# Kernel tuning notes

Measured on AMD Instinct MI355X. Metric: run time of the kernel, lower is better.

Reference implementation:

```python
import jax, jax.numpy as jnp
import numpy as np

HEADS = 4
DIM_K = 16
DIM_U = 1
EPS = 1e-5


def _rel_pos_idx(n):
    # torch: meshgrid(ij) -> stack -> '(i j) n'; rel = pos[None,:]-pos[:,None] + n-1
    ii, jj = np.meshgrid(np.arange(n), np.arange(n), indexing='ij')
    pos = np.stack([ii, jj]).reshape(2, -1).T  # (n*n, 2)
    rel = pos[None, :] - pos[:, None] + (n - 1)  # (N, N, 2)
    return rel[..., 0], rel[..., 1]


def _bn(t, gamma, beta):
    # BatchNorm2d in training mode: batch stats over (b, h, w), biased var
    mu = t.mean(axis=(0, 1, 2))
    var = t.var(axis=(0, 1, 2))
    return (t - mu) * jax.lax.rsqrt(var + EPS) * gamma + beta


def setup_inputs() -> dict:
    key = jax.random.key(0)
    ks = jax.random.split(key, 16)
    b, n, c = 8, 48, 128
    hk = DIM_K * HEADS          # 64
    v = 128 // HEADS            # 32 (dim_out // heads)
    rl = 2 * n - 1              # 95
    s = 0.02
    return {
        'x': jax.random.normal(ks[0], (b, n, n, c), jnp.float32),
        'cor': jax.random.normal(ks[1], (b, n, n, 2), jnp.float32),
        'Wq': jax.random.normal(ks[2], (hk, c), jnp.float32) * s,
        'Wk': jax.random.normal(ks[3], (DIM_K * DIM_U, c), jnp.float32) * s,
        'Wv': jax.random.normal(ks[4], (v * DIM_U, c), jnp.float32) * s,
        'Wce': jax.random.normal(ks[5], (hk, 2), jnp.float32) * s,
        'bce': jax.random.normal(ks[6], (hk,), jnp.float32) * s,
        'Wcc': jax.random.normal(ks[7], (hk, 128), jnp.float32) * s,
        'Wmp': jax.random.normal(ks[8], (128, hk), jnp.float32) * s,
        'bmp': jax.random.normal(ks[9], (128,), jnp.float32) * s,
        'gq': jnp.ones((hk,), jnp.float32),
        'bq': jnp.zeros((hk,), jnp.float32),
        'gv': jnp.ones((v * DIM_U,), jnp.float32),
        'bv': jnp.zeros((v * DIM_U,), jnp.float32),
        'rel_pos_emb': jax.random.normal(ks[10], (rl, rl, DIM_K, DIM_U), jnp.float32),
    }


def reference(x, cor, Wq, Wk, Wv, Wce, bce, Wcc, Wmp, bmp, gq, bq, gv, bv, rel_pos_emb):
    b, hh, ww, c = x.shape
    h, u, kd = HEADS, DIM_U, DIM_K
    vd = Wv.shape[0] // u
    N = hh * ww

    # frame reversal along batch
    x_rev = jnp.concatenate([x[b // 2:], x[:b // 2]], axis=0)

    # 1x1 convs as channel matmuls (channels-last)
    q = jnp.einsum('bhwc,oc->bhwo', x, Wq)
    k = jnp.einsum('bhwc,oc->bhwo', x_rev, Wk)
    v = jnp.einsum('bhwc,oc->bhwo', x_rev, Wv)

    Qn = _bn(q, gq, bq)
    Vn = _bn(v, gv, bv)

    Q = jnp.transpose(Qn.reshape(b, N, h, kd), (0, 2, 3, 1))       # b h k n
    K = jnp.transpose(k.reshape(b, N, u, kd), (0, 2, 3, 1))        # b u k m
    V = jnp.transpose(Vn.reshape(b, N, u, vd), (0, 2, 3, 1))       # b u v m

    K = jax.nn.softmax(K, axis=-1)
    lamc = jnp.einsum('bukm,buvm->bkv', K, V)
    Yc = jnp.einsum('bhkn,bkv->bhvn', Q, lamc)

    # relative position lambda (global branch)
    ni, mi = _rel_pos_idx(hh)
    emb = rel_pos_emb[ni, mi]                                      # n m k u
    lamp = jnp.einsum('nmku,buvm->bnkv', emb, V)
    Yp = jnp.einsum('bhkn,bnkv->bhvn', Q, lamp)

    Y = Yc + Yp                                                    # b h v n
    appearance = jnp.transpose(Y.reshape(b, h, vd, hh, ww), (0, 3, 4, 1, 2)).reshape(b, hh, ww, h * vd)

    cor_embed_ = jnp.einsum('bhwc,oc->bhwo', cor, Wce) + bce       # b hh ww (h k)
    cor_embed = jnp.transpose(cor_embed_.reshape(b, N, h, kd), (0, 2, 3, 1))  # b h k n
    crc = jnp.einsum('bhkn,bkv->bhvn', cor_embed, lamc)
    crp = jnp.einsum('bhkn,bnkv->bhvn', cor_embed, lamp)
    cor_reverse_ = jnp.transpose((crc + crp).reshape(b, h, vd, hh, ww), (0, 3, 4, 1, 2)).reshape(b, hh, ww, h * vd)
    cor_reverse = jnp.einsum('bhwc,oc->bhwo', cor_reverse_, Wcc)
    motion = jnp.einsum('bhwc,oc->bhwo', cor_reverse - cor_embed_, Wmp) + bmp
    return appearance, motion
```

## Files before the change

### kernel.cpp

```cpp
#include <hip/hip_runtime.h>
#include <math.h>
#include <stdint.h>

#define NNPOS 2304
#define ROWS  18432
#define NK    96

#define O_Q   0ul
#define O_K   1179648ul
#define O_V   1474560ul
#define O_ST  2064384ul
#define O_VP  2064704ul
#define O_QP  2457920ul
#define O_LC  4817216ul
#define O_RT  6000960ul
#define O_WG  6148416ul
#define O_B2  6148672ul
#define O_WB  6148800ul
#define O_PT  6155968ul
#define O_PV  6164160ul
#define O_PE  6166208ul
#define O_WFB 6167232ul
#define O_CRF 6175424ul

typedef __bf16 bf16x8 __attribute__((ext_vector_type(8)));
typedef float  f32x4  __attribute__((ext_vector_type(4)));
typedef unsigned int u32;
typedef u32 u32x4 __attribute__((ext_vector_type(4)));

__global__ void k_fold(const float* __restrict__ Wcc, const float* __restrict__ Wce,
                       const float* __restrict__ Wmp, const float* __restrict__ bmp,
                       const float* __restrict__ bce, const float* __restrict__ Wq,
                       const float* __restrict__ Wk, const float* __restrict__ Wv,
                       float* __restrict__ ws) {
  const int t = threadIdx.x;
  const int g = blockIdx.x * 256 + t;
  const int o2 = g >> 7, c = g & 127;
  float acc = 0.f;
#pragma unroll 8
  for (int o = 0; o < 64; ++o) acc += Wmp[o2 * 64 + o] * Wcc[o * 128 + c];
  ((__bf16*)(ws + O_WFB))[o2 * 128 + c] = (__bf16)acc;
  if (blockIdx.x == 0 && t < 128) {
    float a0 = 0.f, a1 = 0.f, ab = 0.f;
#pragma unroll 8
    for (int o = 0; o < 64; ++o) {
      float w = Wmp[t * 64 + o];
      a0 += w * Wce[o * 2]; a1 += w * Wce[o * 2 + 1]; ab += w * bce[o];
    }
    ws[O_WG + t * 2] = a0; ws[O_WG + t * 2 + 1] = a1; ws[O_B2 + t] = bmp[t] - ab;
  }
  __bf16* wbp = (__bf16*)(ws + O_WB);
  if (g < 14336) {
    float w;
    if (g < 8192) w = Wq[g];
    else if (g < 10240) w = Wk[g - 8192];
    else w = Wv[g - 10240];
    wbp[g] = (__bf16)w;
  }
}

__global__ __launch_bounds__(256) void k_qkv(const float* __restrict__ x,
                                             float* __restrict__ ws) {
  const int t = threadIdx.x;
  const int wave = t >> 6, lane = t & 63;
  const int lr = lane & 15, quad = lane >> 4;
  const int r0 = blockIdx.x * 64 + wave * 16;
  const int b = r0 / NNPOS;
  const int n0 = r0 - b * NNPOS;
  const size_t outbase = (size_t)(((b + 4) & 7)) * NNPOS + n0;

  const __bf16* wb = (const __bf16*)(ws + O_WB);
  const float* xrow = x + (size_t)(r0 + lr) * 128;

  f32x4 acc[7];
#pragma unroll
  for (int i = 0; i < 7; ++i) acc[i] = (f32x4){0.f, 0.f, 0.f, 0.f};

#pragma unroll
  for (int ks = 0; ks < 4; ++ks) {
    const float* ap = xrow + ks * 32 + quad * 8;
    float4 a0 = *(const float4*)(ap);
    float4 a1 = *(const float4*)(ap + 4);
    bf16x8 af;
    af[0] = (__bf16)a0.x; af[1] = (__bf16)a0.y; af[2] = (__bf16)a0.z; af[3] = (__bf16)a0.w;
    af[4] = (__bf16)a1.x; af[5] = (__bf16)a1.y; af[6] = (__bf16)a1.z; af[7] = (__bf16)a1.w;
#pragma unroll
    for (int ct = 0; ct < 7; ++ct) {
      bf16x8 bfrag = *(const bf16x8*)(wb + (ct * 16 + lr) * 128 + ks * 32 + quad * 8);
      acc[ct] = __builtin_amdgcn_mfma_f32_16x16x32_bf16(af, bfrag, acc[ct], 0, 0, 0);
    }
  }

#pragma unroll
  for (int ct = 0; ct < 7; ++ct) {
#pragma unroll
    for (int reg = 0; reg < 4; ++reg) {
      int m = quad * 4 + reg;
      int oc = ct * 16 + lr;
      float vvv = acc[ct][reg];
      if (ct < 4)      ws[O_Q + (size_t)(r0 + m) * 64 + oc] = vvv;
      else if (ct < 5) ws[O_K + (outbase + m) * 16 + (oc - 64)] = vvv;
      else             ws[O_V + (outbase + m) * 32 + (oc - 80)] = vvv;
    }
  }
}

__global__ void k_rt(const float* __restrict__ rel, float* __restrict__ ws) {
  __bf16* rt = (__bf16*)(ws + O_RT);
  int i = blockIdx.x * 256 + threadIdx.x;
  if (i < 144400) {
    int kc = i & 15, rr = i >> 4;
    int ri = rr / 95, rj = rr - ri * 95;
    rt[(size_t)kc * 9216 + ri * 96 + rj] = (__bf16)rel[i];
  }
}

__global__ void k_zero(float* __restrict__ ws) {
  __bf16* vp = (__bf16*)(ws + O_VP);
  int i = blockIdx.x * 256 + threadIdx.x;
  if (i < 4096) ws[O_LC + i] = 0.f;
  int bv = i / 96, rem = i - bv * 96;
  int mi = rem >> 1, h8 = rem & 1;
  uint4 z; z.x = 0; z.y = 0; z.z = 0; z.w = 0;
  *(uint4*)(vp + (size_t)bv * 3072 + mi * 64 + 48 + h8 * 8) = z;
}

__global__ void k_zout(float* __restrict__ out, float* __restrict__ ws) {
  size_t i = (size_t)blockIdx.x * 256 + threadIdx.x;
  f32x4 z = {0.f, 0.f, 0.f, 0.f};
  ((f32x4*)out)[i] = z;
  ((f32x4*)(ws + O_CRF))[i] = z;
}

__global__ void k_stats1(float* __restrict__ ws) {
  const int t = threadIdx.x, blk = blockIdx.x;
  __shared__ float sh[512];
  if (blk < 64) {
    const int ch = t & 63, rsub = t >> 6;
    const float* src = ws + O_Q;
    const int r0 = blk * 288;
    float s = 0.f, s2 = 0.f;
#pragma unroll 4
    for (int i = 0; i < 72; ++i) {
      float v = src[(size_t)(r0 + rsub + i * 4) * 64 + ch];
      s += v; s2 += v * v;
    }
    sh[t] = s; sh[256 + t] = s2;
    __syncthreads();
    if (t < 64) {
      float S = sh[t] + sh[t + 64] + sh[t + 128] + sh[t + 192];
      float S2 = sh[256 + t] + sh[256 + t + 64] + sh[256 + t + 128] + sh[256 + t + 192];
      ws[O_PT + blk * 128 + t * 2] = S; ws[O_PT + blk * 128 + t * 2 + 1] = S2;
    }
  } else if (blk < 96) {
    const int j = blk - 64;
    const int ch = t & 31, rsub = t >> 5;
    const float* src = ws + O_V;
    const int r0 = j * 576;
    float s = 0.f, s2 = 0.f;
#pragma unroll 4
    for (int i = 0; i < 72; ++i) {
      float v = src[(size_t)(r0 + rsub + i * 8) * 32 + ch];
      s += v; s2 += v * v;
    }
    sh[t] = s; sh[256 + t] = s2;
    __syncthreads();
    if (t < 32) {
      float S = 0.f, S2 = 0.f;
#pragma unroll
      for (int k = 0; k < 8; ++k) { S += sh[t + k * 32]; S2 += sh[256 + t + k * 32]; }
      ws[O_PV + j * 64 + t * 2] = S; ws[O_PV + j * 64 + t * 2 + 1] = S2;
    }
  } else {
    const int idx = blk - 96;
    const int b = idx >> 3, sl = idx & 7;
    const int kc = t & 15, rsub = t >> 4;
    const int r0 = b * 2304 + sl * 288;
    float s = 0.f;
#pragma unroll 2
    for (int i = 0; i < 18; ++i)
      s += __expf(ws[O_K + (size_t)(r0 + rsub + i * 16) * 16 + kc]);
    sh[t] = s;
    __syncthreads();
    if (t < 16) {
      float S = 0.f;
#pragma unroll
      for (int k = 0; k < 16; ++k) S += sh[t + k * 16];
      ws[O_PE + b * 128 + sl * 16 + t] = S;
    }
  }
}

__global__ void k_stats2(const float* __restrict__ gq, const float* __restrict__ bq,
                         const float* __restrict__ gv, const float* __restrict__ bv,
                         float* __restrict__ ws) {
  const int t = threadIdx.x;
  if (t < 64) {
    float S = 0.f, S2 = 0.f;
    for (int i = 0; i < 64; ++i) { S += ws[O_PT + i * 128 + t * 2]; S2 += ws[O_PT + i * 128 + t * 2 + 1]; }
    float mu = S / 18432.f, var = S2 / 18432.f - mu * mu;
    float sc = gq[t] * rsqrtf(var + 1e-5f);
    ws[O_ST + t] = sc; ws[O_ST + 64 + t] = bq[t] - mu * sc;
  } else if (t < 96) {
    int ch = t - 64;
    float S = 0.f, S2 = 0.f;
    for (int i = 0; i < 32; ++i) { S += ws[O_PV + i * 64 + ch * 2]; S2 += ws[O_PV + i * 64 + ch * 2 + 1]; }
    float mu = S / 18432.f, var = S2 / 18432.f - mu * mu;
    float sc = gv[ch] * rsqrtf(var + 1e-5f);
    ws[O_ST + 128 + ch] = sc; ws[O_ST + 160 + ch] = bv[ch] - mu * sc;
  } else if (t < 224) {
    int idx = t - 96; int b = idx >> 4, kc = idx & 15;
    float S = 0.f;
#pragma unroll
    for (int sl = 0; sl < 8; ++sl) S += ws[O_PE + b * 128 + sl * 16 + kc];
    ws[O_ST + 192 + idx] = 1.f / S;
  }
}

__global__ void k_vp(float* __restrict__ ws) {
  const int b = blockIdx.x / 48, mi = blockIdx.x - b * 48;
  const int t = threadIdx.x;
  __shared__ float Vn[48 * 33];
  const float* st = ws + O_ST;
  const int r0 = b * 2304 + mi * 48;
#pragma unroll
  for (int i = t; i < 1536; i += 256) {
    int r = i >> 5, j = i & 31;
    Vn[r * 33 + j] = ws[O_V + (size_t)(r0 + r) * 32 + j] * st[128 + j] + st[160 + j];
  }
  __syncthreads();
  __bf16* vp = (__bf16*)(ws + O_VP);
  const int j = t >> 3, seg = t & 7;
  unsigned short u[6];
#pragma unroll
  for (int q = 0; q < 6; ++q)
    u[q] = __builtin_bit_cast(unsigned short, (__bf16)Vn[(seg * 6 + q) * 33 + j]);
  u32 w0 = (u32)u[0] | ((u32)u[1] << 16);
  u32 w1 = (u32)u[2] | ((u32)u[3] << 16);
  u32 w2 = (u32)u[4] | ((u32)u[5] << 16);
  u32* dst = (u32*)(vp + (size_t)(b * 32 + j) * 3072 + mi * 64 + seg * 6);
  dst[0] = w0; dst[1] = w1; dst[2] = w2;
}

__global__ void k_prep(const float* __restrict__ cor, const float* __restrict__ Wce,
                       const float* __restrict__ bce, float* __restrict__ ws) {
  const int t = threadIdx.x;
  const int rl = t >> 5, j = t & 31;
  const int rid = blockIdx.x * 8 + rl;
  const int b = rid / NNPOS, n = rid - b * NNPOS;
  const float* st = ws + O_ST;
  float c0 = cor[rid * 2], c1 = cor[rid * 2 + 1];
#pragma unroll
  for (int ch = j; ch < 64; ch += 32) {
    float qn = ws[O_Q + (size_t)rid * 64 + ch] * st[ch] + st[64 + ch];
    ws[O_QP + (size_t)(n * 8 + b) * 128 + ch] = qn;
    float ce = c0 * Wce[ch * 2] + c1 * Wce[ch * 2 + 1] + bce[ch];
    ws[O_QP + (size_t)(n * 8 + b) * 128 + 64 + ch] = ce;
  }
}

__global__ void k_lamc(float* __restrict__ ws) {
  const int b = blockIdx.x / 36, sl = blockIdx.x - b * 36;
  const int t = threadIdx.x;
  __shared__ float eK[16][16];
  __shared__ float Vn[16][33];
  const float* st = ws + O_ST;
  const int kc = t & 15, vp_ = t >> 4;
  const int v0 = vp_ * 2, v1 = v0 + 1;
  float a0 = 0.f, a1 = 0.f;
  const int m0 = b * 2304 + sl * 64;
  const int jj = t & 31, rw = t >> 5;
  const float scj = st[128 + jj], bij = st[160 + jj];
  for (int ch = 0; ch < 4; ++ch) {
    const int mbase = m0 + ch * 16;
    eK[t >> 4][t & 15] = __expf(ws[O_K + (size_t)(mbase + (t >> 4)) * 16 + (t & 15)]);
    Vn[rw][jj]     = ws[O_V + (size_t)(mbase + rw) * 32 + jj] * scj + bij;
    Vn[rw + 8][jj] = ws[O_V + (size_t)(mbase + rw + 8) * 32 + jj] * scj + bij;
    __syncthreads();
#pragma unroll
    for (int m = 0; m < 16; ++m) {
      float e = eK[m][kc];
      a0 += e * Vn[m][v0];
      a1 += e * Vn[m][v1];
    }
    __syncthreads();
  }
  atomicAdd(&ws[O_LC + (size_t)(b * 16 + kc) * 32 + v0], a0);
  atomicAdd(&ws[O_LC + (size_t)(b * 16 + kc) * 32 + v1], a1);
}

__global__ __launch_bounds__(256, 2) void k_lamp(float* __restrict__ ws,
                                                 float* __restrict__ out) {
  __shared__ __align__(16) char smem[33792];
  bf16x8* Bs16 = (bf16x8*)smem;
  u32* Sw = (u32*)(smem + 8192);
  float* Cs = (float*)smem;

  const int t = threadIdx.x;
  const int bx = blockIdx.x;
  const int ni = bx / 6;
  const int sset = bx - ni * 6;
  const int s0 = (sset < 3) ? sset * 16 : (sset - 3) * 16 + 1;
  const int chalf = blockIdx.y;
  const int khalf = blockIdx.z;
  const int ks0 = khalf * 48, ksE = ks0 + 48;
  const int colbase = chalf * 128;
  const int wave = t >> 6, lane = t & 63;
  const int wrow = wave >> 1, wcol = wave & 1;
  const int lr = lane & 15, quad = lane >> 4;

  const __bf16* vp = (const __bf16*)(ws + O_VP);
  const unsigned short* rp = (const unsigned short*)(ws + O_RT);

  const int ia0 = t;
  const int kcA0 = ia0 / 24, wpA0 = ia0 - kcA0 * 24;
  const int ia1 = t + 256;
  const int kcA1 = ia1 / 24, wpA1 = ia1 - kcA1 * 24;
  const bool hasA1 = (ia1 < 384);

  const int colB0 = t >> 2, pB0 = ((t & 3) - ((t >> 3) & 3)) & 3;
  const int ub1 = t + 256;
  const int colB1 = ub1 >> 2, pB1 = ((ub1 & 3) - ((ub1 >> 3) & 3)) & 3;
  const __bf16* gB0 = vp + (size_t)(colbase + colB0) * 3072 + pB0 * 8;
  const __bf16* gB1 = vp + (size_t)(colbase + colB1) * 3072 + pB1 * 8;

  f32x4 acc[4][4];
  {
    f32x4 zz = {0.f, 0.f, 0.f, 0.f};
#pragma unroll
    for (int i = 0; i < 4; ++i)
#pragma unroll
      for (int j = 0; j < 4; ++j) acc[i][j] = zz;
  }

  u32 sa0 = 0, sa1 = 0;
  bf16x8 vb0, vb1;

  auto loadStep = [&](int ksn) {
    const int mi = ksn >> 1, mj0 = (ksn & 1) << 5;
    const int P0 = 96 * (mi - ni + 47) + mj0 - s0 + 33;
    const int k0 = ksn * 32;
    long b0 = (long)kcA0 * 9216 + P0 + 2 * wpA0;
    if (P0 & 1) sa0 = (u32)rp[b0] | ((u32)rp[b0 + 1] << 16);
    else        sa0 = *(const u32*)(rp + b0);
    if (hasA1) {
      long b1 = (long)kcA1 * 9216 + P0 + 2 * wpA1;
      if (P0 & 1) sa1 = (u32)rp[b1] | ((u32)rp[b1 + 1] << 16);
      else        sa1 = *(const u32*)(rp + b1);
    }
    vb0 = *(const bf16x8*)(gB0 + k0);
    vb1 = *(const bf16x8*)(gB1 + k0);
  };

  loadStep(ks0);

  for (int ks = ks0; ks < ksE; ++ks) {
    __syncthreads();
    Sw[kcA0 * 25 + wpA0] = sa0;
    if (hasA1) Sw[kcA1 * 25 + wpA1] = sa1;
    Bs16[t] = vb0;
    Bs16[t + 256] = vb1;
    __syncthreads();

    if (ks + 1 < ksE) loadStep(ks + 1);

    bf16x8 af[4], bfr[4];
#pragma unroll
    for (int rt = 0; rt < 4; ++rt) {
      int nl = wrow * 4 + rt;
      int wb = lr * 25 + (7 - nl) + quad * 4;
      u32x4 dd = { Sw[wb], Sw[wb + 1], Sw[wb + 2], Sw[wb + 3] };
      af[rt] = __builtin_bit_cast(bf16x8, dd);
    }
#pragma unroll
    for (int ct = 0; ct < 4; ++ct) {
      int col = wcol * 64 + ct * 16 + lr;
      int u = col * 4 + ((quad + (col >> 1)) & 3);
      bfr[ct] = Bs16[u];
    }
#pragma unroll
    for (int rt = 0; rt < 4; ++rt)
#pragma unroll
      for (int ct = 0; ct < 4; ++ct)
        acc[rt][ct] = __builtin_amdgcn_mfma_f32_16x16x32_bf16(af[rt], bfr[ct], acc[rt][ct], 0, 0, 0);
  }

  const float* lamcp = ws + O_LC;
  const float* Qp = ws + O_QP;
  float* crf = ws + O_CRF;
  const int s = t >> 5, vv = t & 31;

  for (int h = 0; h < 2; ++h) {
    __syncthreads();
    if (wrow == h) {
#pragma unroll
      for (int rt = 0; rt < 4; ++rt) {
#pragma unroll
        for (int ct = 0; ct < 4; ++ct) {
          int col = wcol * 64 + ct * 16 + lr;
          int bb = chalf * 4 + (col >> 5);
          int vl = col & 31;
#pragma unroll
          for (int reg = 0; reg < 4; ++reg) {
            int row = rt * 16 + quad * 4 + reg;
            int kc = row & 15;
            float add = 0.f;
            if (khalf == 0) {
              float dinv = ws[O_ST + 192 + bb * 16 + kc];
              add = lamcp[(bb * 16 + kc) * 32 + vl] * dinv;
            }
            Cs[row * 132 + col] = acc[rt][ct][reg] + add;
          }
        }
      }
    }
    __syncthreads();
#pragma unroll
    for (int i = 0; i < 16; ++i) {
      int combo = s * 16 + i;
      int hp = combo & 7, bl = (combo >> 3) & 3, nr = combo >> 5;
      int n = ni * 48 + s0 + 2 * (h * 4 + nr);
      int bb = chalf * 4 + bl;
      const float* qrow = Qp + ((size_t)(n * 8 + bb) * 8 + hp) * 16;
      const float* crow = Cs + (nr * 16) * 132 + bl * 32 + vv;
      float y = 0.f;
#pragma unroll
      for (int kc = 0; kc < 16; ++kc) y += qrow[kc] * crow[kc * 132];
      size_t idx = (size_t)(bb * NNPOS + n) * 128 + (hp & 3) * 32 + vv;
      if (hp < 4) atomicAdd(&out[idx], y);
      else        atomicAdd(&crf[idx], y);
    }
  }
}

__global__ __launch_bounds__(256) void k_motion(const float* __restrict__ cor,
                                                float* __restrict__ ws,
                                                float* __restrict__ out) {
  const int t = threadIdx.x;
  const int wave = t >> 6, lane = t & 63;
  const int lr = lane & 15, quad = lane >> 4;
  const int r0 = blockIdx.x * 64 + wave * 16;
  const float* crf = ws + O_CRF;
  const __bf16* wfb = (const __bf16*)(ws + O_WFB);

  f32x4 acc[8];
#pragma unroll
  for (int i = 0; i < 8; ++i) acc[i] = (f32x4){0.f, 0.f, 0.f, 0.f};

#pragma unroll
  for (int ks = 0; ks < 4; ++ks) {
    const float* ap = crf + (size_t)(r0 + lr) * 128 + ks * 32 + quad * 8;
    float4 a0 = *(const float4*)(ap);
    float4 a1 = *(const float4*)(ap + 4);
    bf16x8 af;
    af[0] = (__bf16)a0.x; af[1] = (__bf16)a0.y; af[2] = (__bf16)a0.z; af[3] = (__bf16)a0.w;
    af[4] = (__bf16)a1.x; af[5] = (__bf16)a1.y; af[6] = (__bf16)a1.z; af[7] = (__bf16)a1.w;
#pragma unroll
    for (int ct = 0; ct < 8; ++ct) {
      bf16x8 bfrag = *(const bf16x8*)(wfb + (ct * 16 + lr) * 128 + ks * 32 + quad * 8);
      acc[ct] = __builtin_amdgcn_mfma_f32_16x16x32_bf16(af, bfrag, acc[ct], 0, 0, 0);
    }
  }

#pragma unroll
  for (int reg = 0; reg < 4; ++reg) {
    int row = r0 + quad * 4 + reg;
    float c0 = cor[row * 2], c1 = cor[row * 2 + 1];
#pragma unroll
    for (int ct = 0; ct < 8; ++ct) {
      int o2 = ct * 16 + lr;
      float y = acc[ct][reg] + ws[O_B2 + o2] - c0 * ws[O_WG + o2 * 2] - c1 * ws[O_WG + o2 * 2 + 1];
      out[2359296ul + (size_t)row * 128 + o2] = y;
    }
  }
}

extern "C" void kernel_launch(void* const* d_in, const int* in_sizes, int n_in,
                              void* d_out, int out_size, void* d_ws, size_t ws_size,
                              hipStream_t stream) {
  const float* x   = (const float*)d_in[0];
  const float* cor = (const float*)d_in[1];
  const float* Wq  = (const float*)d_in[2];
  const float* Wk  = (const float*)d_in[3];
  const float* Wv  = (const float*)d_in[4];
  const float* Wce = (const float*)d_in[5];
  const float* bce = (const float*)d_in[6];
  const float* Wcc = (const float*)d_in[7];
  const float* Wmp = (const float*)d_in[8];
  const float* bmp = (const float*)d_in[9];
  const float* gq  = (const float*)d_in[10];
  const float* bq  = (const float*)d_in[11];
  const float* gv  = (const float*)d_in[12];
  const float* bv  = (const float*)d_in[13];
  const float* rel = (const float*)d_in[14];
  float* out = (float*)d_out;
  float* ws  = (float*)d_ws;

  k_fold  <<<64, 256, 0, stream>>>(Wcc, Wce, Wmp, bmp, bce, Wq, Wk, Wv, ws);
  k_qkv   <<<288, 256, 0, stream>>>(x, ws);
  k_rt    <<<565, 256, 0, stream>>>(rel, ws);
  k_zero  <<<96, 256, 0, stream>>>(ws);
  k_zout  <<<2304, 256, 0, stream>>>(out, ws);
  k_stats1<<<160, 256, 0, stream>>>(ws);
  k_stats2<<<1, 256, 0, stream>>>(gq, bq, gv, bv, ws);
  k_vp    <<<384, 256, 0, stream>>>(ws);
  k_lamc  <<<288, 256, 0, stream>>>(ws);
  k_prep  <<<2304, 256, 0, stream>>>(cor, Wce, bce, ws);
  k_lamp  <<<dim3(288, 2, 2), 256, 0, stream>>>(ws, out);
  k_motion<<<288, 256, 0, stream>>>(cor, ws, out);
}
```

Measured before the change: 252.8 us.

## Merge setup kernels and load relative-position A fragments directly from global

Measured after the change: 347.4 us. 1.37x slower.

```diff
diff --git a/kernel.cpp b/kernel.cpp
--- a/kernel.cpp
+++ b/kernel.cpp
@@ -27,35 +27,63 @@
 typedef float  f32x4  __attribute__((ext_vector_type(4)));
 typedef unsigned int u32;
 typedef u32 u32x4 __attribute__((ext_vector_type(4)));
-
-__global__ void k_fold(const float* __restrict__ Wcc, const float* __restrict__ Wce,
-                       const float* __restrict__ Wmp, const float* __restrict__ bmp,
-                       const float* __restrict__ bce, const float* __restrict__ Wq,
-                       const float* __restrict__ Wk, const float* __restrict__ Wv,
-                       float* __restrict__ ws) {
-  const int t = threadIdx.x;
-  const int g = blockIdx.x * 256 + t;
-  const int o2 = g >> 7, c = g & 127;
-  float acc = 0.f;
+struct __attribute__((packed, aligned(4))) bf16x8p { bf16x8 v; };
+
+__global__ void k_pre(const float* __restrict__ Wcc, const float* __restrict__ Wce,
+                      const float* __restrict__ Wmp, const float* __restrict__ bmp,
+                      const float* __restrict__ bce, const float* __restrict__ Wq,
+                      const float* __restrict__ Wk, const float* __restrict__ Wv,
+                      const float* __restrict__ rel,
+                      float* __restrict__ out, float* __restrict__ ws) {
+  const int t = threadIdx.x, blk = blockIdx.x;
+  if (blk < 64) {
+    const int g = blk * 256 + t;
+    const int o2 = g >> 7, c = g & 127;
+    float acc = 0.f;
 #pragma unroll 8
-  for (int o = 0; o < 64; ++o) acc += Wmp[o2 * 64 + o] * Wcc[o * 128 + c];
-  ((__bf16*)(ws + O_WFB))[o2 * 128 + c] = (__bf16)acc;
-  if (blockIdx.x == 0 && t < 128) {
-    float a0 = 0.f, a1 = 0.f, ab = 0.f;
+    for (int o = 0; o < 64; ++o) acc += Wmp[o2 * 64 + o] * Wcc[o * 128 + c];
+    ((__bf16*)(ws + O_WFB))[o2 * 128 + c] = (__bf16)acc;
+    if (blk == 0 && t < 128) {
+      float a0 = 0.f, a1 = 0.f, ab = 0.f;
 #pragma unroll 8
-    for (int o = 0; o < 64; ++o) {
-      float w = Wmp[t * 64 + o];
-      a0 += w * Wce[o * 2]; a1 += w * Wce[o * 2 + 1]; ab += w * bce[o];
-    }
-    ws[O_WG + t * 2] = a0; ws[O_WG + t * 2 + 1] = a1; ws[O_B2 + t] = bmp[t] - ab;
-  }
-  __bf16* wbp = (__bf16*)(ws + O_WB);
-  if (g < 14336) {
-    float w;
-    if (g < 8192) w = Wq[g];
-    else if (g < 10240) w = Wk[g - 8192];
-    else w = Wv[g - 10240];
-    wbp[g] = (__bf16)w;
+      for (int o = 0; o < 64; ++o) {
+        float w = Wmp[t * 64 + o];
+        a0 += w * Wce[o * 2]; a1 += w * Wce[o * 2 + 1]; ab += w * bce[o];
+      }
+      ws[O_WG + t * 2] = a0; ws[O_WG + t * 2 + 1] = a1; ws[O_B2 + t] = bmp[t] - ab;
+    }
+    __bf16* wbp = (__bf16*)(ws + O_WB);
+    if (g < 14336) {
+      float w;
+      if (g < 8192) w = Wq[g];
+      else if (g < 10240) w = Wk[g - 8192];
+      else w = Wv[g - 10240];
+      wbp[g] = (__bf16)w;
+    }
+  } else if (blk < 629) {
+    __bf16* rt = (__bf16*)(ws + O_RT);
+    int i = (blk - 64) * 256 + t;
+    if (i < 144400) {
+      int kc = i & 15, rr = i >> 4;
+      int ri = rr / 95, rj = rr - ri * 95;
+      int d = ri * 96 + rj;
+      __bf16 v = (__bf16)rel[i];
+      rt[(size_t)kc * 9216 + d] = v;
+      if (d > 0) rt[147456ul + (size_t)kc * 9216 + d - 1] = v;
+    }
+  } else if (blk < 725) {
+    __bf16* vp = (__bf16*)(ws + O_VP);
+    int i = (blk - 629) * 256 + t;
+    if (i < 4096) ws[O_LC + i] = 0.f;
+    int bv = i / 96, rem = i - bv * 96;
+    int mi = rem >> 1, h8 = rem & 1;
+    uint4 z; z.x = 0; z.y = 0; z.z = 0; z.w = 0;
+    *(uint4*)(vp + (size_t)bv * 3072 + mi * 64 + 48 + h8 * 8) = z;
+  } else {
+    size_t i = (size_t)(blk - 725) * 256 + t;
+    f32x4 z = {0.f, 0.f, 0.f, 0.f};
+    ((f32x4*)out)[i] = z;
+    ((f32x4*)(ws + O_CRF))[i] = z;
   }
 }
 
@@ -103,33 +131,6 @@
       else             ws[O_V + (outbase + m) * 32 + (oc - 80)] = vvv;
     }
   }
-}
-
-__global__ void k_rt(const float* __restrict__ rel, float* __restrict__ ws) {
-  __bf16* rt = (__bf16*)(ws + O_RT);
-  int i = blockIdx.x * 256 + threadIdx.x;
-  if (i < 144400) {
-    int kc = i & 15, rr = i >> 4;
-    int ri = rr / 95, rj = rr - ri * 95;
-    rt[(size_t)kc * 9216 + ri * 96 + rj] = (__bf16)rel[i];
-  }
-}
-
-__global__ void k_zero(float* __restrict__ ws) {
-  __bf16* vp = (__bf16*)(ws + O_VP);
-  int i = blockIdx.x * 256 + threadIdx.x;
-  if (i < 4096) ws[O_LC + i] = 0.f;
-  int bv = i / 96, rem = i - bv * 96;
-  int mi = rem >> 1, h8 = rem & 1;
-  uint4 z; z.x = 0; z.y = 0; z.z = 0; z.w = 0;
-  *(uint4*)(vp + (size_t)bv * 3072 + mi * 64 + 48 + h8 * 8) = z;
-}
-
-__global__ void k_zout(float* __restrict__ out, float* __restrict__ ws) {
-  size_t i = (size_t)blockIdx.x * 256 + threadIdx.x;
-  f32x4 z = {0.f, 0.f, 0.f, 0.f};
-  ((f32x4*)out)[i] = z;
-  ((f32x4*)(ws + O_CRF))[i] = z;
 }
 
 __global__ void k_stats1(float* __restrict__ ws) {
@@ -217,83 +218,77 @@
   }
 }
 
-__global__ void k_vp(float* __restrict__ ws) {
-  const int b = blockIdx.x / 48, mi = blockIdx.x - b * 48;
-  const int t = threadIdx.x;
-  __shared__ float Vn[48 * 33];
+__global__ void k_mid(const float* __restrict__ cor, const float* __restrict__ Wce,
+                      const float* __restrict__ bce, float* __restrict__ ws) {
+  const int t = threadIdx.x, blk = blockIdx.x;
+  __shared__ float shm[48 * 33];
   const float* st = ws + O_ST;
-  const int r0 = b * 2304 + mi * 48;
-#pragma unroll
-  for (int i = t; i < 1536; i += 256) {
-    int r = i >> 5, j = i & 31;
-    Vn[r * 33 + j] = ws[O_V + (size_t)(r0 + r) * 32 + j] * st[128 + j] + st[160 + j];
-  }
-  __syncthreads();
-  __bf16* vp = (__bf16*)(ws + O_VP);
-  const int j = t >> 3, seg = t & 7;
-  unsigned short u[6];
-#pragma unroll
-  for (int q = 0; q < 6; ++q)
-    u[q] = __builtin_bit_cast(unsigned short, (__bf16)Vn[(seg * 6 + q) * 33 + j]);
-  u32 w0 = (u32)u[0] | ((u32)u[1] << 16);
-  u32 w1 = (u32)u[2] | ((u32)u[3] << 16);
-  u32 w2 = (u32)u[4] | ((u32)u[5] << 16);
-  u32* dst = (u32*)(vp + (size_t)(b * 32 + j) * 3072 + mi * 64 + seg * 6);
-  dst[0] = w0; dst[1] = w1; dst[2] = w2;
-}
-
-__global__ void k_prep(const float* __restrict__ cor, const float* __restrict__ Wce,
-                       const float* __restrict__ bce, float* __restrict__ ws) {
-  const int t = threadIdx.x;
-  const int rl = t >> 5, j = t & 31;
-  const int rid = blockIdx.x * 8 + rl;
-  const int b = rid / NNPOS, n = rid - b * NNPOS;
-  const float* st = ws + O_ST;
-  float c0 = cor[rid * 2], c1 = cor[rid * 2 + 1];
-#pragma unroll
-  for (int ch = j; ch < 64; ch += 32) {
-    float qn = ws[O_Q + (size_t)rid * 64 + ch] * st[ch] + st[64 + ch];
-    ws[O_QP + (size_t)(n * 8 + b) * 128 + ch] = qn;
-    float ce = c0 * Wce[ch * 2] + c1 * Wce[ch * 2 + 1] + bce[ch];
-    ws[O_QP + (size_t)(n * 8 + b) * 128 + 64 + ch] = ce;
-  }
-}
-
-__global__ void k_lamc(float* __restrict__ ws) {
-  const int b = blockIdx.x / 36, sl = blockIdx.x - b * 36;
-  const int t = threadIdx.x;
-  __shared__ float eK[16][16];
-  __shared__ float Vn[16][33];
-  const float* st = ws + O_ST;
-  const int kc = t & 15, vp_ = t >> 4;
-  const int v0 = vp_ * 2, v1 = v0 + 1;
-  float a0 = 0.f, a1 = 0.f;
-  const int m0 = b * 2304 + sl * 64;
-  const int jj = t & 31, rw = t >> 5;
-  const float scj = st[128 + jj], bij = st[160 + jj];
-  for (int ch = 0; ch < 4; ++ch) {
-    const int mbase = m0 + ch * 16;
-    eK[t >> 4][t & 15] = __expf(ws[O_K + (size_t)(mbase + (t >> 4)) * 16 + (t & 15)]);
-    Vn[rw][jj]     = ws[O_V + (size_t)(mbase + rw) * 32 + jj] * scj + bij;
-    Vn[rw + 8][jj] = ws[O_V + (size_t)(mbase + rw + 8) * 32 + jj] * scj + bij;
-    __syncthreads();
-#pragma unroll
-    for (int m = 0; m < 16; ++m) {
-      float e = eK[m][kc];
-      a0 += e * Vn[m][v0];
-      a1 += e * Vn[m][v1];
-    }
-    __syncthreads();
-  }
-  atomicAdd(&ws[O_LC + (size_t)(b * 16 + kc) * 32 + v0], a0);
-  atomicAdd(&ws[O_LC + (size_t)(b * 16 + kc) * 32 + v1], a1);
-}
-
-__global__ __launch_bounds__(256, 2) void k_lamp(float* __restrict__ ws,
+  if (blk < 384) {
+    const int b = blk / 48, mi = blk - b * 48;
+    const int r0 = b * 2304 + mi * 48;
+#pragma unroll
+    for (int i = t; i < 1536; i += 256) {
+      int r = i >> 5, j = i & 31;
+      shm[r * 33 + j] = ws[O_V + (size_t)(r0 + r) * 32 + j] * st[128 + j] + st[160 + j];
+    }
+    __syncthreads();
+    __bf16* vp = (__bf16*)(ws + O_VP);
+    const int j = t >> 3, seg = t & 7;
+    unsigned short u[6];
+#pragma unroll
+    for (int q = 0; q < 6; ++q)
+      u[q] = __builtin_bit_cast(unsigned short, (__bf16)shm[(seg * 6 + q) * 33 + j]);
+    u32 w0 = (u32)u[0] | ((u32)u[1] << 16);
+    u32 w1 = (u32)u[2] | ((u32)u[3] << 16);
+    u32 w2 = (u32)u[4] | ((u32)u[5] << 16);
+    u32* dst = (u32*)(vp + (size_t)(b * 32 + j) * 3072 + mi * 64 + seg * 6);
+    dst[0] = w0; dst[1] = w1; dst[2] = w2;
+  } else if (blk < 672) {
+    const int idx = blk - 384;
+    const int b = idx / 36, sl = idx - b * 36;
+    float* eK = shm;
+    float* Vn = shm + 256;
+    const int kc = t & 15, vp_ = t >> 4;
+    const int v0 = vp_ * 2, v1 = v0 + 1;
+    float a0 = 0.f, a1 = 0.f;
+    const int m0 = b * 2304 + sl * 64;
+    const int jj = t & 31, rw = t >> 5;
+    const float scj = st[128 + jj], bij = st[160 + jj];
+    for (int ch = 0; ch < 4; ++ch) {
+      const int mbase = m0 + ch * 16;
+      eK[(t >> 4) * 16 + (t & 15)] = __expf(ws[O_K + (size_t)(mbase + (t >> 4)) * 16 + (t & 15)]);
+      Vn[rw * 33 + jj]       = ws[O_V + (size_t)(mbase + rw) * 32 + jj] * scj + bij;
+      Vn[(rw + 8) * 33 + jj] = ws[O_V + (size_t)(mbase + rw + 8) * 32 + jj] * scj + bij;
+      __syncthreads();
+#pragma unroll
+      for (int m = 0; m < 16; ++m) {
+        float e = eK[m * 16 + kc];
+        a0 += e * Vn[m * 33 + v0];
+        a1 += e * Vn[m * 33 + v1];
+      }
+      __syncthreads();
+    }
+    atomicAdd(&ws[O_LC + (size_t)(b * 16 + kc) * 32 + v0], a0);
+    atomicAdd(&ws[O_LC + (size_t)(b * 16 + kc) * 32 + v1], a1);
+  } else {
+    const int rl = t >> 5, j = t & 31;
+    const int rid = (blk - 672) * 8 + rl;
+    const int b = rid / NNPOS, n = rid - b * NNPOS;
+    float c0 = cor[rid * 2], c1 = cor[rid * 2 + 1];
+#pragma unroll
+    for (int ch = j; ch < 64; ch += 32) {
+      float qn = ws[O_Q + (size_t)rid * 64 + ch] * st[ch] + st[64 + ch];
+      ws[O_QP + (size_t)(n * 8 + b) * 128 + ch] = qn;
+      float ce = c0 * Wce[ch * 2] + c1 * Wce[ch * 2 + 1] + bce[ch];
+      ws[O_QP + (size_t)(n * 8 + b) * 128 + 64 + ch] = ce;
+    }
+  }
+}
+
+__global__ __launch_bounds__(256, 4) void k_lamp(float* __restrict__ ws,
                                                  float* __restrict__ out) {
   __shared__ __align__(16) char smem[33792];
   bf16x8* Bs16 = (bf16x8*)smem;
-  u32* Sw = (u32*)(smem + 8192);
   float* Cs = (float*)smem;
 
   const int t = threadIdx.x;
@@ -310,13 +305,11 @@
   const int lr = lane & 15, quad = lane >> 4;
 
   const __bf16* vp = (const __bf16*)(ws + O_VP);
-  const unsigned short* rp = (const unsigned short*)(ws + O_RT);
-
-  const int ia0 = t;
-  const int kcA0 = ia0 / 24, wpA0 = ia0 - kcA0 * 24;
-  const int ia1 = t + 256;
-  const int kcA1 = ia1 / 24, wpA1 = ia1 - kcA1 * 24;
-  const bool hasA1 = (ia1 < 384);
+
+  const int parity = (s0 + 1) & 1;
+  const unsigned short* rpA = (const unsigned short*)(ws + O_RT) +
+                              (size_t)parity * 147456 + (size_t)lr * 9216 +
+                              (47 - parity - s0 + quad * 8 - 8 * wrow);
 
   const int colB0 = t >> 2, pB0 = ((t & 3) - ((t >> 3) & 3)) & 3;
   const int ub1 = t + 256;
@@ -333,56 +326,48 @@
       for (int j = 0; j < 4; ++j) acc[i][j] = zz;
   }
 
-  u32 sa0 = 0, sa1 = 0;
-  bf16x8 vb0, vb1;
-
-  auto loadStep = [&](int ksn) {
+  bf16x8 afC[4], afN[4], vb0, vb1;
+
+  auto loadA = [&](int ksn, bf16x8* dst) {
     const int mi = ksn >> 1, mj0 = (ksn & 1) << 5;
-    const int P0 = 96 * (mi - ni + 47) + mj0 - s0 + 33;
+    const unsigned short* p = rpA + (96 * (mi - ni + 47) + mj0);
+#pragma unroll
+    for (int rt = 0; rt < 4; ++rt)
+      dst[rt] = ((const bf16x8p*)(p - 2 * rt))->v;
+  };
+  auto loadB = [&](int ksn) {
     const int k0 = ksn * 32;
-    long b0 = (long)kcA0 * 9216 + P0 + 2 * wpA0;
-    if (P0 & 1) sa0 = (u32)rp[b0] | ((u32)rp[b0 + 1] << 16);
-    else        sa0 = *(const u32*)(rp + b0);
-    if (hasA1) {
-      long b1 = (long)kcA1 * 9216 + P0 + 2 * wpA1;
-      if (P0 & 1) sa1 = (u32)rp[b1] | ((u32)rp[b1 + 1] << 16);
-      else        sa1 = *(const u32*)(rp + b1);
-    }
     vb0 = *(const bf16x8*)(gB0 + k0);
     vb1 = *(const bf16x8*)(gB1 + k0);
   };
 
-  loadStep(ks0);
+  loadB(ks0);
+  loadA(ks0, afC);
 
   for (int ks = ks0; ks < ksE; ++ks) {
     __syncthreads();
-    Sw[kcA0 * 25 + wpA0] = sa0;
-    if (hasA1) Sw[kcA1 * 25 + wpA1] = sa1;
     Bs16[t] = vb0;
     Bs16[t + 256] = vb1;
     __syncthreads();
 
-    if (ks + 1 < ksE) loadStep(ks + 1);
-
-    bf16x8 af[4], bfr[4];
-#pragma unroll
-    for (int rt = 0; rt < 4; ++rt) {
-      int nl = wrow * 4 + rt;
-      int wb = lr * 25 + (7 - nl) + quad * 4;
-      u32x4 dd = { Sw[wb], Sw[wb + 1], Sw[wb + 2], Sw[wb + 3] };
-      af[rt] = __builtin_bit_cast(bf16x8, dd);
-    }
+    if (ks + 1 < ksE) { loadB(ks + 1); loadA(ks + 1, afN); }
+
+    bf16x8 bfr[4];
 #pragma unroll
     for (int ct = 0; ct < 4; ++ct) {
       int col = wcol * 64 + ct * 16 + lr;
-      int u = col * 4 + ((quad + (col >> 1)) & 3);
-      bfr[ct] = Bs16[u];
+      bfr[ct] = Bs16[col * 4 + ((quad + (col >> 1)) & 3)];
     }
 #pragma unroll
     for (int rt = 0; rt < 4; ++rt)
 #pragma unroll
       for (int ct = 0; ct < 4; ++ct)
-        acc[rt][ct] = __builtin_amdgcn_mfma_f32_16x16x32_bf16(af[rt], bfr[ct], acc[rt][ct], 0, 0, 0);
+        acc[rt][ct] = __builtin_amdgcn_mfma_f32_16x16x32_bf16(afC[rt], bfr[ct], acc[rt][ct], 0, 0, 0);
+
+    if (ks + 1 < ksE) {
+#pragma unroll
+      for (int i = 0; i < 4; ++i) afC[i] = afN[i];
+    }
   }
 
   const float* lamcp = ws + O_LC;
@@ -496,16 +481,11 @@
   float* out = (float*)d_out;
   float* ws  = (float*)d_ws;
 
-  k_fold  <<<64, 256, 0, stream>>>(Wcc, Wce, Wmp, bmp, bce, Wq, Wk, Wv, ws);
+  k_pre   <<<3029, 256, 0, stream>>>(Wcc, Wce, Wmp, bmp, bce, Wq, Wk, Wv, rel, out, ws);
   k_qkv   <<<288, 256, 0, stream>>>(x, ws);
-  k_rt    <<<565, 256, 0, stream>>>(rel, ws);
-  k_zero  <<<96, 256, 0, stream>>>(ws);
-  k_zout  <<<2304, 256, 0, stream>>>(out, ws);
   k_stats1<<<160, 256, 0, stream>>>(ws);
   k_stats2<<<1, 256, 0, stream>>>(gq, bq, gv, bv, ws);
-  k_vp    <<<384, 256, 0, stream>>>(ws);
-  k_lamc  <<<288, 256, 0, stream>>>(ws);
-  k_prep  <<<2304, 256, 0, stream>>>(cor, Wce, bce, ws);
+  k_mid   <<<2976, 256, 0, stream>>>(cor, Wce, bce, ws);
   k_lamp  <<<dim3(288, 2, 2), 256, 0, stream>>>(ws, out);
   k_motion<<<288, 256, 0, stream>>>(cor, ws, out);
 }
```
